# Kernel optimization log

Measured on AMD Instinct MI355X. Metric: run time of the kernel, lower is better.

Reference implementation:

```python
import jax, jax.numpy as jnp
import numpy as np

N = 50000
D = 128
E = 600000
C = 128  # out_channels


def setup_inputs() -> dict:
    key = jax.random.key(0)
    ks = jax.random.split(key, 8)
    x = jax.random.normal(ks[0], (N, D), dtype=jnp.float32)
    edge_index = jax.random.randint(ks[1], (2, E), 0, N, dtype=jnp.int64)
    s = 1.0 / np.sqrt(D)
    # layer 1: PyG GraphConv = lin_rel (with bias) on aggregated neighbors + lin_root (no bias) on self
    W1_rel = jax.random.uniform(ks[2], (C, D), jnp.float32, -s, s)
    b1_rel = jax.random.uniform(ks[3], (C,), jnp.float32, -s, s)
    W1_root = jax.random.uniform(ks[4], (C, D), jnp.float32, -s, s)
    s2 = 1.0 / np.sqrt(C)
    W2_rel = jax.random.uniform(ks[5], (C, C), jnp.float32, -s2, s2)
    b2_rel = jax.random.uniform(ks[6], (C,), jnp.float32, -s2, s2)
    W2_root = jax.random.uniform(ks[7], (C, C), jnp.float32, -s2, s2)
    return {"x": x, "edge_index": edge_index,
            "W1_rel": W1_rel, "b1_rel": b1_rel, "W1_root": W1_root,
            "W2_rel": W2_rel, "b2_rel": b2_rel, "W2_root": W2_root}


def _graph_conv(x, src, tgt, W_rel, b_rel, W_root):
    # sum-aggregate source-node features onto targets, then linear transforms
    agg = jax.ops.segment_sum(x[src], tgt, num_segments=N)  # [N, d_in]
    return agg @ W_rel.T + b_rel + x @ W_root.T


def reference(x, edge_index, W1_rel, b1_rel, W1_root, W2_rel, b2_rel, W2_root):
    src, tgt = edge_index[0], edge_index[1]
    h = jax.nn.relu(_graph_conv(x, src, tgt, W1_rel, b1_rel, W1_root))
    h = jax.nn.relu(_graph_conv(h, src, tgt, W2_rel, b2_rel, W2_root))
    return h
```

## Files before the change

### kernel.cpp

```cpp
#include <hip/hip_runtime.h>
#include <hip/hip_bf16.h>

#define DD 128
#define STRIDE 32

typedef __attribute__((ext_vector_type(8))) short bf16x8;
typedef __attribute__((ext_vector_type(4))) float f32x4;
typedef __attribute__((ext_vector_type(8))) unsigned short us8;
typedef __attribute__((ext_vector_type(4))) unsigned short us4;
typedef unsigned short ushort_t;
typedef unsigned int uint_t;

__device__ inline ushort_t f2bf(float f) {
    __hip_bfloat16 h = __float2bfloat16(f);
    union { __hip_bfloat16 h; ushort_t u; } cv;
    cv.h = h;
    return cv.u;
}
__device__ inline float bf2f(uint_t lo16) {
    union { uint_t i; float f; } v;
    v.i = lo16 << 16;
    return v.f;
}
__device__ inline void conv8(const float* __restrict__ in, ushort_t* __restrict__ outp) {
    const float4 va = *(const float4*)in;
    const float4 vb = *(const float4*)(in + 4);
    ushort_t r[8];
    r[0] = f2bf(va.x); r[1] = f2bf(va.y); r[2] = f2bf(va.z); r[3] = f2bf(va.w);
    r[4] = f2bf(vb.x); r[5] = f2bf(vb.y); r[6] = f2bf(vb.z); r[7] = f2bf(vb.w);
    *(bf16x8*)outp = *(bf16x8*)r;
}


__global__ __launch_bounds__(256) void prep_small(int* __restrict__ pos, int n4, int zb,
                                                  ushort_t* __restrict__ esrc, int pb,
                                                  ushort_t* __restrict__ xb,
                                                  ushort_t* __restrict__ aggb, int n) {
    const int blk = blockIdx.x;
    if (blk < zb) {
        int i = blk * 256 + threadIdx.x;
        if (i < n4) ((int4*)pos)[i] = make_int4(0, 0, 0, 0);
    } else if (blk < zb + pb) {
        int i = (blk - zb) * 256 + threadIdx.x;
        if (i < n * (STRIDE / 8)) {
            us8 f;
#pragma unroll
            for (int k = 0; k < 8; ++k) f[k] = (ushort_t)n;
            ((us8*)esrc)[i] = f;
        }
    } else {
        int t = threadIdx.x;
        if (t < 64)       ((uint_t*)(xb + (size_t)n * DD))[t] = 0u;
        else if (t < 128) ((uint_t*)(aggb + (size_t)n * DD))[t - 64] = 0u;
    }
}


__global__ __launch_bounds__(256) void scatter_conv(const int* __restrict__ tgt,
                                                    const int* __restrict__ src,
                                                    int* __restrict__ pos,
                                                    ushort_t* __restrict__ esrc, int e, int eb,
                                                    const float* __restrict__ x,
                                                    ushort_t* __restrict__ xb, int n8, int xcb,
                                                    const float* __restrict__ a,
                                                    const float* __restrict__ b,
                                                    const float* __restrict__ c,
                                                    const float* __restrict__ d,
                                                    ushort_t* __restrict__ wb) {
    const int blk = blockIdx.x;
    if (blk < eb) {
        int i = blk * 256 + threadIdx.x;
        int e8 = e >> 3;
        if (i < e8) {
            int4 t0 = ((const int4*)tgt)[i * 2];
            int4 t1 = ((const int4*)tgt)[i * 2 + 1];
            int4 s0 = ((const int4*)src)[i * 2];
            int4 s1 = ((const int4*)src)[i * 2 + 1];
            int r0 = atomicAdd(&pos[t0.x], 1) & (STRIDE - 1);
            int r1 = atomicAdd(&pos[t0.y], 1) & (STRIDE - 1);
            int r2 = atomicAdd(&pos[t0.z], 1) & (STRIDE - 1);
            int r3 = atomicAdd(&pos[t0.w], 1) & (STRIDE - 1);
            int r4 = atomicAdd(&pos[t1.x], 1) & (STRIDE - 1);
            int r5 = atomicAdd(&pos[t1.y], 1) & (STRIDE - 1);
            int r6 = atomicAdd(&pos[t1.z], 1) & (STRIDE - 1);
            int r7 = atomicAdd(&pos[t1.w], 1) & (STRIDE - 1);
            esrc[t0.x * STRIDE + r0] = (ushort_t)s0.x;
            esrc[t0.y * STRIDE + r1] = (ushort_t)s0.y;
            esrc[t0.z * STRIDE + r2] = (ushort_t)s0.z;
            esrc[t0.w * STRIDE + r3] = (ushort_t)s0.w;
            esrc[t1.x * STRIDE + r4] = (ushort_t)s1.x;
            esrc[t1.y * STRIDE + r5] = (ushort_t)s1.y;
            esrc[t1.z * STRIDE + r6] = (ushort_t)s1.z;
            esrc[t1.w * STRIDE + r7] = (ushort_t)s1.w;
        }
        if (i == 0)
            for (int j = e8 * 8; j < e; ++j) {
                int t = tgt[j];
                int r = atomicAdd(&pos[t], 1) & (STRIDE - 1);
                esrc[t * STRIDE + r] = (ushort_t)src[j];
            }
    } else if (blk < eb + xcb) {
        int i = (blk - eb) * 256 + threadIdx.x;
        if (i < n8) conv8(x + (size_t)i * 8, xb + (size_t)i * 8);
    } else {
        int k = (blk - eb - xcb) * 256 + threadIdx.x;
        if (k >= 8192) return;
        const float* p = (k < 2048) ? a : (k < 4096) ? b : (k < 6144) ? c : d;
        conv8(p + (size_t)(k & 2047) * 8, wb + (size_t)k * 8);
    }
}


__global__ __launch_bounds__(256) void gather_agg_bf16(const ushort_t* __restrict__ xin,
                                                       const int* __restrict__ pos,
                                                       const ushort_t* __restrict__ esrc,
                                                       ushort_t* __restrict__ agg, int n) {
    const int lane = threadIdx.x & 63;
    const int node = blockIdx.x * 4 + (threadIdx.x >> 6);
    if (node >= n) return;
    int deg = pos[node];
    deg = deg > STRIDE ? STRIDE : deg;
    const int epochs = (deg + 15) >> 4;
    const int grp = lane >> 4;
    const int l16 = lane & 15;
    const ushort_t* bktg = esrc + (size_t)node * STRIDE + grp * 4;
    const ushort_t* xcol = xin + l16 * 8;
    float acc[8];
#pragma unroll
    for (int c = 0; c < 8; ++c) acc[c] = 0.f;

    for (int ep = 0; ep < epochs; ++ep) {
        us4 idv = *(const us4*)(bktg + ep * 16);
        bf16x8 v0 = *(const bf16x8*)(xcol + (size_t)idv[0] * DD);
        bf16x8 v1 = *(const bf16x8*)(xcol + (size_t)idv[1] * DD);
        bf16x8 v2 = *(const bf16x8*)(xcol + (size_t)idv[2] * DD);
        bf16x8 v3 = *(const bf16x8*)(xcol + (size_t)idv[3] * DD);
#pragma unroll
        for (int c = 0; c < 8; ++c) {
            acc[c] += bf2f((ushort_t)v0[c]) + bf2f((ushort_t)v1[c])
                    + bf2f((ushort_t)v2[c]) + bf2f((ushort_t)v3[c]);
        }
    }
#pragma unroll
    for (int c = 0; c < 8; ++c) {
        acc[c] += __shfl_xor(acc[c], 16, 64);
        acc[c] += __shfl_xor(acc[c], 32, 64);
    }
    if (lane < 16) {
        ushort_t r[8];
#pragma unroll
        for (int c = 0; c < 8; ++c) r[c] = f2bf(acc[c]);
        *(bf16x8*)(agg + (size_t)node * DD + l16 * 8) = *(bf16x8*)r;
    }
}

template<bool OUT_BF16>
__global__ __launch_bounds__(256) void gemm_mfma(
    const ushort_t* Aagg, const ushort_t* __restrict__ Aroot,
    const ushort_t* __restrict__ Wrel, const ushort_t* __restrict__ Wroot,
    const float* __restrict__ bias, void* outv, int n)
{
    const int wave = threadIdx.x >> 6;
    const int lane = threadIdx.x & 63;
    const int m = lane & 15;
    const int kg = lane >> 4;
    const int rbase = blockIdx.x * 64 + wave * 16;
    if (rbase >= n) return;
    const size_t aoff = (size_t)(rbase + m) * DD + kg * 8;

    f32x4 acc[8];
#pragma unroll
    for (int j = 0; j < 8; ++j) acc[j] = (f32x4){0.f, 0.f, 0.f, 0.f};

#pragma unroll
    for (int k0 = 0; k0 < DD; k0 += 32) {
        bf16x8 aA = *(const bf16x8*)(Aagg + aoff + k0);
        bf16x8 aR = *(const bf16x8*)(Aroot + aoff + k0);
#pragma unroll
        for (int j = 0; j < 8; ++j) {
            bf16x8 bL = *(const bf16x8*)(Wrel + (size_t)(j * 16 + m) * DD + kg * 8 + k0);
            bf16x8 bR = *(const bf16x8*)(Wroot + (size_t)(j * 16 + m) * DD + kg * 8 + k0);
            acc[j] = __builtin_amdgcn_mfma_f32_16x16x32_bf16(aA, bL, acc[j], 0, 0, 0);
            acc[j] = __builtin_amdgcn_mfma_f32_16x16x32_bf16(aR, bR, acc[j], 0, 0, 0);
        }
    }

    const int orow = rbase + kg * 4;
#pragma unroll
    for (int j = 0; j < 8; ++j) {
        const int col = j * 16 + m;
        const float bv = bias[col];
#pragma unroll
        for (int i = 0; i < 4; ++i) {
            float v = acc[j][i] + bv;
            v = v > 0.f ? v : 0.f;
            if (OUT_BF16)
                ((ushort_t*)outv)[(size_t)(orow + i) * DD + col] = f2bf(v);
            else
                ((float*)outv)[(size_t)(orow + i) * DD + col] = v;
        }
    }
}

extern "C" void kernel_launch(void* const* d_in, const int* in_sizes, int n_in,
                              void* d_out, int out_size, void* d_ws, size_t ws_size,
                              hipStream_t stream) {
    const float* x = (const float*)d_in[0];
    const int* ei = (const int*)d_in[1];
    const float* W1rel = (const float*)d_in[2];
    const float* b1 = (const float*)d_in[3];
    const float* W1root = (const float*)d_in[4];
    const float* W2rel = (const float*)d_in[5];
    const float* b2 = (const float*)d_in[6];
    const float* W2root = (const float*)d_in[7];
    float* out = (float*)d_out;

    const int n = in_sizes[0] / DD;
    const int e = in_sizes[1] / 2;
    const int* src = ei;
    const int* tgt = ei + e;
    const int n8 = n * DD / 8;
    const int zb = (n / 4 + 255) / 256;
    const int xcb = (n8 + 255) / 256;
    const int pb = (n * (STRIDE / 8) + 255) / 256;
    const int eb = (e / 8 + 255) / 256;

    char* ws = (char*)d_ws;
    int* pos = (int*)ws;
    ushort_t* wb = (ushort_t*)(ws + 200064);
    ushort_t* esrc = (ushort_t*)(ws + 331136);
    ushort_t* aggb = (ushort_t*)(ws + 3531264);
    ushort_t* xb = (ushort_t*)(ws + 16331776);

    prep_small<<<zb + pb + 1, 256, 0, stream>>>(pos, n / 4, zb, esrc, pb, xb, aggb, n);
    scatter_conv<<<eb + xcb + 32, 256, 0, stream>>>(tgt, src, pos, esrc, e, eb,
                                                    x, xb, n8, xcb,
                                                    W1rel, W1root, W2rel, W2root, wb);

    gather_agg_bf16<<<(n + 3) / 4, 256, 0, stream>>>(xb, pos, esrc, aggb, n);
    gemm_mfma<true><<<(n + 63) / 64, 256, 0, stream>>>(aggb, xb, wb, wb + 16384, b1, aggb, n);

    gather_agg_bf16<<<(n + 3) / 4, 256, 0, stream>>>(aggb, pos, esrc, xb, n);
    gemm_mfma<false><<<(n + 63) / 64, 256, 0, stream>>>(xb, aggb, wb + 32768, wb + 49152, b2, out, n);
}
```

Baseline: 161.5 us.

## Replace global per-node atomics with two-pass binned edge bucketing

Edge bucketing now runs in two passes instead of one global atomicAdd per edge on per-node counters. First, each block counts edges per 256-node bin in LDS, reserves space with one global atomic per bin, and writes packed (local node, src) words into fixed-size bin regions. A new finalize kernel then builds the per-node slot lists and degrees with LDS atomics. This cuts global atomic traffic but adds a kernel launch and an extra pass over roughly 2.4MB of binned data. Bins are capped at 4096 entries and the 256-entry cursor array limits it to about 65K nodes.

```diff
diff --git a/kernel.cpp b/kernel.cpp
--- a/kernel.cpp
+++ b/kernel.cpp
@@ -3,6 +3,8 @@
 
 #define DD 128
 #define STRIDE 32
+#define BINSZ 4096
+#define EPB 2048
 
 typedef __attribute__((ext_vector_type(8))) short bf16x8;
 typedef __attribute__((ext_vector_type(4))) float f32x4;
@@ -32,22 +34,21 @@
 }
 
 
-__global__ __launch_bounds__(256) void prep_small(int* __restrict__ pos, int n4, int zb,
-                                                  ushort_t* __restrict__ esrc, int pb,
+__global__ __launch_bounds__(256) void prep_small(ushort_t* __restrict__ esrc, int pb,
+                                                  int* __restrict__ binCursor,
                                                   ushort_t* __restrict__ xb,
                                                   ushort_t* __restrict__ aggb, int n) {
     const int blk = blockIdx.x;
-    if (blk < zb) {
+    if (blk < pb) {
         int i = blk * 256 + threadIdx.x;
-        if (i < n4) ((int4*)pos)[i] = make_int4(0, 0, 0, 0);
-    } else if (blk < zb + pb) {
-        int i = (blk - zb) * 256 + threadIdx.x;
         if (i < n * (STRIDE / 8)) {
             us8 f;
 #pragma unroll
             for (int k = 0; k < 8; ++k) f[k] = (ushort_t)n;
             ((us8*)esrc)[i] = f;
         }
+    } else if (blk == pb) {
+        binCursor[threadIdx.x] = 0;
     } else {
         int t = threadIdx.x;
         if (t < 64)       ((uint_t*)(xb + (size_t)n * DD))[t] = 0u;
@@ -56,49 +57,67 @@
 }
 
 
-__global__ __launch_bounds__(256) void scatter_conv(const int* __restrict__ tgt,
-                                                    const int* __restrict__ src,
-                                                    int* __restrict__ pos,
-                                                    ushort_t* __restrict__ esrc, int e, int eb,
-                                                    const float* __restrict__ x,
-                                                    ushort_t* __restrict__ xb, int n8, int xcb,
-                                                    const float* __restrict__ a,
-                                                    const float* __restrict__ b,
-                                                    const float* __restrict__ c,
-                                                    const float* __restrict__ d,
-                                                    ushort_t* __restrict__ wb) {
+__global__ __launch_bounds__(256) void bin_scatter_conv(
+    const int* __restrict__ tgt, const int* __restrict__ src,
+    int* __restrict__ binCursor, uint_t* __restrict__ binReg, int e, int eb,
+    const float* __restrict__ x, ushort_t* __restrict__ xb, int n8, int xcb,
+    const float* __restrict__ a, const float* __restrict__ b,
+    const float* __restrict__ c, const float* __restrict__ d,
+    ushort_t* __restrict__ wb)
+{
     const int blk = blockIdx.x;
     if (blk < eb) {
-        int i = blk * 256 + threadIdx.x;
-        int e8 = e >> 3;
-        if (i < e8) {
-            int4 t0 = ((const int4*)tgt)[i * 2];
-            int4 t1 = ((const int4*)tgt)[i * 2 + 1];
-            int4 s0 = ((const int4*)src)[i * 2];
-            int4 s1 = ((const int4*)src)[i * 2 + 1];
-            int r0 = atomicAdd(&pos[t0.x], 1) & (STRIDE - 1);
-            int r1 = atomicAdd(&pos[t0.y], 1) & (STRIDE - 1);
-            int r2 = atomicAdd(&pos[t0.z], 1) & (STRIDE - 1);
-            int r3 = atomicAdd(&pos[t0.w], 1) & (STRIDE - 1);
-            int r4 = atomicAdd(&pos[t1.x], 1) & (STRIDE - 1);
-            int r5 = atomicAdd(&pos[t1.y], 1) & (STRIDE - 1);
-            int r6 = atomicAdd(&pos[t1.z], 1) & (STRIDE - 1);
-            int r7 = atomicAdd(&pos[t1.w], 1) & (STRIDE - 1);
-            esrc[t0.x * STRIDE + r0] = (ushort_t)s0.x;
-            esrc[t0.y * STRIDE + r1] = (ushort_t)s0.y;
-            esrc[t0.z * STRIDE + r2] = (ushort_t)s0.z;
-            esrc[t0.w * STRIDE + r3] = (ushort_t)s0.w;
-            esrc[t1.x * STRIDE + r4] = (ushort_t)s1.x;
-            esrc[t1.y * STRIDE + r5] = (ushort_t)s1.y;
-            esrc[t1.z * STRIDE + r6] = (ushort_t)s1.z;
-            esrc[t1.w * STRIDE + r7] = (ushort_t)s1.w;
-        }
-        if (i == 0)
-            for (int j = e8 * 8; j < e; ++j) {
-                int t = tgt[j];
-                int r = atomicAdd(&pos[t], 1) & (STRIDE - 1);
-                esrc[t * STRIDE + r] = (ushort_t)src[j];
+        __shared__ int lcnt[256];
+        __shared__ int lbase[256];
+        const int tid = threadIdx.x;
+        lcnt[tid] = 0;
+        __syncthreads();
+
+        const int ebase = blk * EPB + tid * 8;
+        const bool valid = (ebase + 8 <= e);
+        int tg[8], sr[8], bn[8];
+        if (valid) {
+            int4 t0 = ((const int4*)tgt)[ebase / 4];
+            int4 t1 = ((const int4*)tgt)[ebase / 4 + 1];
+            int4 s0 = ((const int4*)src)[ebase / 4];
+            int4 s1 = ((const int4*)src)[ebase / 4 + 1];
+            tg[0] = t0.x; tg[1] = t0.y; tg[2] = t0.z; tg[3] = t0.w;
+            tg[4] = t1.x; tg[5] = t1.y; tg[6] = t1.z; tg[7] = t1.w;
+            sr[0] = s0.x; sr[1] = s0.y; sr[2] = s0.z; sr[3] = s0.w;
+            sr[4] = s1.x; sr[5] = s1.y; sr[6] = s1.z; sr[7] = s1.w;
+#pragma unroll
+            for (int k = 0; k < 8; ++k) {
+                bn[k] = tg[k] >> 8;
+                atomicAdd(&lcnt[bn[k]], 1);
             }
+        }
+        __syncthreads();
+        {
+            int c0 = lcnt[tid];
+            int gb = (c0 > 0) ? atomicAdd(&binCursor[tid], c0) : 0;
+            lbase[tid] = gb;
+            lcnt[tid] = 0;
+        }
+        __syncthreads();
+        if (valid) {
+#pragma unroll
+            for (int k = 0; k < 8; ++k) {
+                int r = atomicAdd(&lcnt[bn[k]], 1);
+                int slot = lbase[bn[k]] + r;
+                if (slot > BINSZ - 1) slot = BINSZ - 1;
+                binReg[(size_t)bn[k] * BINSZ + slot] =
+                    ((uint_t)(tg[k] & 255) << 16) | (uint_t)sr[k];
+            }
+        }
+        if (blk == 0 && tid == 0) {
+            for (int j = e & ~7; j < e; ++j) {
+                int t = tgt[j], b2 = t >> 8;
+                int slot = atomicAdd(&binCursor[b2], 1);
+                if (slot > BINSZ - 1) slot = BINSZ - 1;
+                binReg[(size_t)b2 * BINSZ + slot] =
+                    ((uint_t)(t & 255) << 16) | (uint_t)src[j];
+            }
+        }
     } else if (blk < eb + xcb) {
         int i = (blk - eb) * 256 + threadIdx.x;
         if (i < n8) conv8(x + (size_t)i * 8, xb + (size_t)i * 8);
@@ -107,6 +126,33 @@
         if (k >= 8192) return;
         const float* p = (k < 2048) ? a : (k < 4096) ? b : (k < 6144) ? c : d;
         conv8(p + (size_t)(k & 2047) * 8, wb + (size_t)k * 8);
+    }
+}
+
+
+__global__ __launch_bounds__(256) void bin_finalize(const int* __restrict__ binCursor,
+                                                    const uint_t* __restrict__ binReg,
+                                                    ushort_t* __restrict__ esrc,
+                                                    int* __restrict__ pos, int n) {
+    const int bin = blockIdx.x;
+    const int tid = threadIdx.x;
+    __shared__ int cnt[256];
+    cnt[tid] = 0;
+    __syncthreads();
+    int total = binCursor[bin];
+    if (total > BINSZ) total = BINSZ;
+    const uint_t* reg = binReg + (size_t)bin * BINSZ;
+    for (int i = tid; i < total; i += 256) {
+        uint_t p = reg[i];
+        int node = p >> 16;
+        int r = atomicAdd(&cnt[node], 1) & (STRIDE - 1);
+        esrc[(size_t)(bin * 256 + node) * STRIDE + r] = (ushort_t)(p & 0xffffu);
+    }
+    __syncthreads();
+    int node = bin * 256 + tid;
+    if (node < n) {
+        int dg = cnt[tid];
+        pos[node] = dg > STRIDE ? STRIDE : dg;
     }
 }
 
@@ -220,22 +266,25 @@
     const int* src = ei;
     const int* tgt = ei + e;
     const int n8 = n * DD / 8;
-    const int zb = (n / 4 + 255) / 256;
     const int xcb = (n8 + 255) / 256;
     const int pb = (n * (STRIDE / 8) + 255) / 256;
-    const int eb = (e / 8 + 255) / 256;
+    const int eb = (e + EPB - 1) / EPB;
+    const int nbins = (n + 255) >> 8;
 
     char* ws = (char*)d_ws;
     int* pos = (int*)ws;
-    ushort_t* wb = (ushort_t*)(ws + 200064);
-    ushort_t* esrc = (ushort_t*)(ws + 331136);
-    ushort_t* aggb = (ushort_t*)(ws + 3531264);
-    ushort_t* xb = (ushort_t*)(ws + 16331776);
-
-    prep_small<<<zb + pb + 1, 256, 0, stream>>>(pos, n / 4, zb, esrc, pb, xb, aggb, n);
-    scatter_conv<<<eb + xcb + 32, 256, 0, stream>>>(tgt, src, pos, esrc, e, eb,
-                                                    x, xb, n8, xcb,
-                                                    W1rel, W1root, W2rel, W2root, wb);
+    int* binCursor = (int*)(ws + 200064);
+    ushort_t* wb = (ushort_t*)(ws + 201088);
+    ushort_t* esrc = (ushort_t*)(ws + 332160);
+    uint_t* binReg = (uint_t*)(ws + 3532160);
+    ushort_t* aggb = (ushort_t*)(ws + 6743424);
+    ushort_t* xb = (ushort_t*)(ws + 19543680);
+
+    prep_small<<<pb + 2, 256, 0, stream>>>(esrc, pb, binCursor, xb, aggb, n);
+    bin_scatter_conv<<<eb + xcb + 32, 256, 0, stream>>>(
+        tgt, src, binCursor, binReg, e, eb, x, xb, n8, xcb,
+        W1rel, W1root, W2rel, W2root, wb);
+    bin_finalize<<<nbins, 256, 0, stream>>>(binCursor, binReg, esrc, pos, n);
 
     gather_agg_bf16<<<(n + 3) / 4, 256, 0, stream>>>(xb, pos, esrc, aggb, n);
     gemm_mfma<true><<<(n + 63) / 64, 256, 0, stream>>>(aggb, xb, wb, wb + 16384, b1, aggb, n);
```

After: 143.2 us. 1.13x faster.
